# Kernel optimization log

Hardware: AMD Instinct MI355X
Metric: run time of the kernel (lower is better)

## Reference

```python
import jax, jax.numpy as jnp
import numpy as np

B, S, E, H = 1, 4096, 768, 12
D = E // H  # head_dim = 64


def setup_inputs() -> dict:
    key = jax.random.key(0)
    ks = jax.random.split(key, 6)
    scale = 0.02
    x = jax.random.normal(ks[0], (B, S, E), dtype=jnp.float32)
    Wq = jax.random.normal(ks[1], (E, E), dtype=jnp.float32) * scale
    Wk = jax.random.normal(ks[2], (E, E), dtype=jnp.float32) * scale
    Wv = jax.random.normal(ks[3], (E, E), dtype=jnp.float32) * scale
    Wo = jax.random.normal(ks[4], (E, E), dtype=jnp.float32) * scale
    bo = jax.random.normal(ks[5], (E,), dtype=jnp.float32) * scale
    mask = jnp.tril(jnp.ones((S, S), dtype=bool))[None, None]  # [1,1,S,S] causal
    return {"x": x, "Wq": Wq, "Wk": Wk, "Wv": Wv, "Wo": Wo, "bo": bo, "mask": mask}


def reference(x, Wq, Wk, Wv, Wo, bo, mask):
    # projections (torch Linear: y = x @ W.T; here W stored as [E,E] applied as x@W)
    q = jnp.einsum('bse,ef->bsf', x, Wq).reshape(B, S, H, D).transpose(0, 2, 1, 3)
    k = jnp.einsum('bse,ef->bsf', x, Wk).reshape(B, S, H, D).transpose(0, 2, 1, 3)
    v = jnp.einsum('bse,ef->bsf', x, Wv).reshape(B, S, H, D).transpose(0, 2, 1, 3)
    scores = jnp.einsum('bhqd,bhkd->bhqk', q, k) / jnp.sqrt(jnp.float32(D))
    scores = jnp.where(mask, scores, -jnp.inf)
    attn = jax.nn.softmax(scores, axis=-1)  # dropout p=0 -> identity
    ctx = jnp.einsum('bhqk,bhkd->bhqd', attn, v)
    ctx = ctx.transpose(0, 2, 1, 3).reshape(B, S, E)
    return jnp.einsum('bse,ef->bsf', ctx, Wo) + bo
```

## Files before the change

### kernel.cpp

```cpp
#include <hip/hip_runtime.h>
#include <math.h>

#define S 4096
#define E 768
#define H 12
#define Dh 64
#define SCALE2 0.1803368801111204f

typedef short short8 __attribute__((ext_vector_type(8)));
typedef float floatx4 __attribute__((ext_vector_type(4)));

__device__ __forceinline__ unsigned short f2bf(float f) {
    union { float f; unsigned int i; } c; c.f = f;
    unsigned int i = c.i;
    return (unsigned short)((i + 0x7fffu + ((i >> 16) & 1u)) >> 16);
}

__device__ __forceinline__ unsigned int pk_bf16(float lo, float hi) {
#if __has_builtin(__builtin_amdgcn_cvt_pk_bf16_f32)
    typedef __bf16 bf16x2 __attribute__((ext_vector_type(2)));
    union { bf16x2 v; unsigned int u; } c;
    c.v = __builtin_amdgcn_cvt_pk_bf16_f32(lo, hi);
    return c.u;
#else
    union { float f; unsigned int i; } a, b; a.f = lo; b.f = hi;
    return ((a.i + 0x8000u) >> 16) | ((b.i + 0x8000u) & 0xFFFF0000u);
#endif
}

__device__ __forceinline__ unsigned int scale_pk(unsigned int u, float s) {
    union { unsigned int i; float f; } lo, hi;
    lo.i = u << 16; hi.i = u & 0xffff0000u;
    return pk_bf16(lo.f * s, hi.f * s);
}

__device__ __forceinline__ void pk_atomic_add_bf16(unsigned short* addr, unsigned int bits) {
    unsigned long long a = (unsigned long long)addr;
    asm volatile("global_atomic_pk_add_bf16 %0, %1, off" :: "v"(a), "v"(bits) : "memory");
}

__device__ __forceinline__ void gload_lds16(const unsigned short* g, unsigned short* l) {
    __builtin_amdgcn_global_load_lds(
        (const __attribute__((address_space(1))) unsigned int*)g,
        (__attribute__((address_space(3))) unsigned int*)l, 16, 0, 0);
}

__device__ __forceinline__ void pl32swap(unsigned &a, unsigned &b) {
#if __has_builtin(__builtin_amdgcn_permlane32_swap)
    typedef unsigned uint2v __attribute__((ext_vector_type(2)));
    uint2v r = __builtin_amdgcn_permlane32_swap(a, b, false, false);
    a = r[0]; b = r[1];
#else
    asm("s_nop 1\n\tv_permlane32_swap_b32 %0, %1\n\ts_nop 1" : "+v"(a), "+v"(b));
#endif
}
__device__ __forceinline__ void pl16swap(unsigned &a, unsigned &b) {
#if __has_builtin(__builtin_amdgcn_permlane16_swap)
    typedef unsigned uint2v __attribute__((ext_vector_type(2)));
    uint2v r = __builtin_amdgcn_permlane16_swap(a, b, false, false);
    a = r[0]; b = r[1];
#else
    asm("s_nop 1\n\tv_permlane16_swap_b32 %0, %1\n\ts_nop 1" : "+v"(a), "+v"(b));
#endif
}

__device__ __forceinline__ short8 quad_redist(unsigned a0, unsigned a1, unsigned a2, unsigned a3) {
    pl32swap(a0, a2); pl16swap(a0, a2);
    pl32swap(a1, a3); pl16swap(a1, a3);
    union { unsigned u[4]; short8 s; } r;
    r.u[0] = a0; r.u[1] = a1; r.u[2] = a2; r.u[3] = a3;
    return r.s;
}

__global__ __launch_bounds__(256)
void prep_kernel(const float* __restrict__ x, unsigned short* __restrict__ xb,
                 const float* __restrict__ s0, const float* __restrict__ s1,
                 const float* __restrict__ s2, const float* __restrict__ s3,
                 unsigned short* __restrict__ d0, unsigned short* __restrict__ d1,
                 unsigned short* __restrict__ d2, unsigned short* __restrict__ d3,
                 char* __restrict__ zbase) {
    __shared__ unsigned short tile[32][33];
    const int b = blockIdx.x;
    const int tid = threadIdx.x;
    if (b < 2304) {
        int z = b / 576, rem = b - z * 576;
        int bx = rem % 24, by = rem / 24;
        const float* src = (z == 0) ? s0 : (z == 1) ? s1 : (z == 2) ? s2 : s3;
        unsigned short* dst = (z == 0) ? d0 : (z == 1) ? d1 : (z == 2) ? d2 : d3;
        int tx = tid & 31, ty = tid >> 5;
        int xcol = bx * 32 + tx;
        int y0 = by * 32;
        for (int j = ty; j < 32; j += 8)
            tile[j][tx] = f2bf(src[(size_t)(y0 + j) * E + xcol]);
        __syncthreads();
        int x2 = y0 + tx;
        int y2 = bx * 32;
        for (int j = ty; j < 32; j += 8)
            dst[(size_t)(y2 + j) * E + x2] = tile[tx][j];
    } else if (b < 3840) {
        int i = ((b - 2304) * 256 + tid) * 8;
        float4 f0 = *reinterpret_cast<const float4*>(x + i);
        float4 f1 = *reinterpret_cast<const float4*>(x + i + 4);
        unsigned short u[8];
        u[0]=f2bf(f0.x); u[1]=f2bf(f0.y); u[2]=f2bf(f0.z); u[3]=f2bf(f0.w);
        u[4]=f2bf(f1.x); u[5]=f2bf(f1.y); u[6]=f2bf(f1.z); u[7]=f2bf(f1.w);
        *reinterpret_cast<uint4*>(xb + i) = *reinterpret_cast<uint4*>(u);
    } else {
        size_t i = (size_t)(b - 3840) * 16384 + (size_t)tid * 64;
        uint4 z4 = make_uint4(0u, 0u, 0u, 0u);
        *reinterpret_cast<uint4*>(zbase + i)      = z4;
        *reinterpret_cast<uint4*>(zbase + i + 16) = z4;
        *reinterpret_cast<uint4*>(zbase + i + 32) = z4;
        *reinterpret_cast<uint4*>(zbase + i + 48) = z4;
    }
}

__global__ __launch_bounds__(256)
void gemm_qkv(const unsigned short* __restrict__ A,
              const unsigned short* __restrict__ BT,
              unsigned short* __restrict__ Qb, unsigned short* __restrict__ Kb,
              unsigned short* __restrict__ VTb) {
    __shared__ unsigned short Asm[128 * 64];
    __shared__ unsigned short Bsm[128 * 64];
    const int tid  = threadIdx.x;
    const int wave = tid >> 6, lane = tid & 63;
    const int quad = lane >> 4, l16 = lane & 15;
    const int lrow = lane >> 3, lchunk = lane & 7;
    const int bb = blockIdx.x;
    const int xcd = bb & 7, j = bb >> 3;
    const int mt = (xcd >> 1) * 8 + (j & 7);
    const int nt = (xcd & 1) * 9 + (j >> 3);
    const int n0 = nt * 128;
    const int m0 = mt * 128;
    const int aw = wave >> 1, bw = wave & 1;

    floatx4 acc[4][4];
    #pragma unroll
    for (int at = 0; at < 4; at++)
        #pragma unroll
        for (int ct = 0; ct < 4; ct++)
            #pragma unroll
            for (int r = 0; r < 4; r++) acc[at][ct][r] = 0.f;

    for (int k0 = 0; k0 < E; k0 += 64) {
        #pragma unroll
        for (int i = 0; i < 4; i++) {
            int rbase = wave * 32 + i * 8;
            int row   = rbase + lrow;
            int gc    = lchunk ^ (row & 7);
            gload_lds16(&A [(size_t)(m0 + row) * E + k0 + gc * 8], &Asm[rbase * 64]);
            gload_lds16(&BT[(size_t)(n0 + row) * E + k0 + gc * 8], &Bsm[rbase * 64]);
        }
        __syncthreads();
        #pragma unroll
        for (int kk = 0; kk < 2; kk++) {
            const int g = kk * 4 + quad;
            short8 af[4], bfr[4];
            #pragma unroll
            for (int t = 0; t < 4; t++) {
                int ar = aw * 64 + t * 16 + l16;
                af[t]  = *reinterpret_cast<const short8*>(&Asm[ar * 64 + (g ^ (ar & 7)) * 8]);
                int br = bw * 64 + t * 16 + l16;
                bfr[t] = *reinterpret_cast<const short8*>(&Bsm[br * 64 + (g ^ (br & 7)) * 8]);
            }
            #pragma unroll
            for (int at = 0; at < 4; at++)
                #pragma unroll
                for (int ct = 0; ct < 4; ct++)
                    acc[at][ct] = __builtin_amdgcn_mfma_f32_16x16x32_bf16(af[at], bfr[ct], acc[at][ct], 0, 0, 0);
        }
        __syncthreads();
    }

    const int sec = n0 / 768;
    const int nb  = n0 - sec * 768 + bw * 64;
    if (sec == 2) {
        #pragma unroll
        for (int at = 0; at < 4; at++)
            #pragma unroll
            for (int ct = 0; ct < 4; ct++) {
                int nsec = nb + ct * 16 + l16, hh = nsec >> 6, d = nsec & 63;
                int s0i = m0 + aw * 64 + at * 16 + quad * 4;
                uint2 w2;
                w2.x = pk_bf16(acc[at][ct][0], acc[at][ct][1]);
                w2.y = pk_bf16(acc[at][ct][2], acc[at][ct][3]);
                *reinterpret_cast<uint2*>(&VTb[(size_t)hh * Dh * S + (size_t)d * S + s0i]) = w2;
            }
    } else {
        #pragma unroll
        for (int at = 0; at < 4; at++)
            #pragma unroll
            for (int ct = 0; ct < 4; ct++) {
                int nsec = nb + ct * 16 + l16, hh = nsec >> 6, d = nsec & 63;
                #pragma unroll
                for (int r = 0; r < 4; r++) {
                    int s = m0 + aw * 64 + at * 16 + quad * 4 + r;
                    float v = acc[at][ct][r];
                    if (sec == 0) Qb[(size_t)hh * S * Dh + (size_t)s * Dh + d] = f2bf(v * SCALE2);
                    else          Kb[(size_t)hh * S * Dh + (size_t)s * Dh + d] = f2bf(v);
                }
            }
    }
}

__global__ __launch_bounds__(256)
void gemm_out(const unsigned short* __restrict__ ctxp,
              const unsigned short* __restrict__ BT,
              const float* __restrict__ lsumf,
              float* __restrict__ outp, const float* __restrict__ bias) {
    __shared__ unsigned short Asm[128 * 64];
    __shared__ unsigned short Bsm[64 * 64];
    const int tid  = threadIdx.x;
    const int wave = tid >> 6, lane = tid & 63;
    const int quad = lane >> 4, l16 = lane & 15;
    const int lrow = lane >> 3, lchunk = lane & 7;
    const int bb = blockIdx.x;
    const int xcd = bb & 7, j = bb >> 3;
    const int mt = (xcd >> 1) * 8 + (j & 7);
    const int nt = (xcd & 1) * 6 + (j >> 3);
    const int n0 = nt * 64;
    const int m0 = mt * 128;
    const int arow = tid >> 1, ahalf = tid & 1;

    floatx4 acc[2][4];
    #pragma unroll
    for (int at = 0; at < 2; at++)
        #pragma unroll
        for (int ct = 0; ct < 4; ct++)
            #pragma unroll
            for (int r = 0; r < 4; r++) acc[at][ct][r] = 0.f;

    for (int k0 = 0; k0 < E; k0 += 64) {
        {
            const unsigned short* asrc = ctxp + (size_t)(m0 + arow) * E + k0 + ahalf * 32;
            float linv = 1.0f / lsumf[(k0 >> 6) * S + m0 + arow];
            #pragma unroll
            for (int cc = 0; cc < 4; cc++) {
                uint4 u = *reinterpret_cast<const uint4*>(asrc + cc * 8);
                uint4 w;
                w.x = scale_pk(u.x, linv);
                w.y = scale_pk(u.y, linv);
                w.z = scale_pk(u.z, linv);
                w.w = scale_pk(u.w, linv);
                int chunk = ahalf * 4 + cc;
                *reinterpret_cast<uint4*>(&Asm[arow * 64 + (chunk ^ (arow & 7)) * 8]) = w;
            }
        }
        #pragma unroll
        for (int i = 0; i < 2; i++) {
            int rbase = wave * 16 + i * 8;
            int row   = rbase + lrow;
            int gc    = lchunk ^ (row & 7);
            gload_lds16(&BT[(size_t)(n0 + row) * E + k0 + gc * 8], &Bsm[rbase * 64]);
        }
        __syncthreads();
        #pragma unroll
        for (int kk = 0; kk < 2; kk++) {
            const int g = kk * 4 + quad;
            short8 af[2], bfr[4];
            #pragma unroll
            for (int t = 0; t < 2; t++) {
                int ar = wave * 32 + t * 16 + l16;
                af[t] = *reinterpret_cast<const short8*>(&Asm[ar * 64 + (g ^ (ar & 7)) * 8]);
            }
            #pragma unroll
            for (int ct = 0; ct < 4; ct++) {
                int br = ct * 16 + l16;
                bfr[ct] = *reinterpret_cast<const short8*>(&Bsm[br * 64 + (g ^ (br & 7)) * 8]);
            }
            #pragma unroll
            for (int at = 0; at < 2; at++)
                #pragma unroll
                for (int ct = 0; ct < 4; ct++)
                    acc[at][ct] = __builtin_amdgcn_mfma_f32_16x16x32_bf16(af[at], bfr[ct], acc[at][ct], 0, 0, 0);
        }
        __syncthreads();
    }

    #pragma unroll
    for (int at = 0; at < 2; at++)
        #pragma unroll
        for (int ct = 0; ct < 4; ct++) {
            int n = n0 + ct * 16 + l16;
            float bn = bias[n];
            #pragma unroll
            for (int r = 0; r < 4; r++) {
                int s = m0 + wave * 32 + at * 16 + quad * 4 + r;
                outp[(size_t)s * E + n] = acc[at][ct][r] + bn;
            }
        }
}

__global__ __launch_bounds__(512, 4)
void attn_kernel(const unsigned short* __restrict__ Q,
                 const unsigned short* __restrict__ K,
                 const unsigned short* __restrict__ VT,
                 unsigned short* __restrict__ ctxp,
                 float* __restrict__ lsumf) {
    __shared__ unsigned short Ksm[3][64 * 64];
    __shared__ unsigned short Vsm[3][64 * 64];
    const int tid  = threadIdx.x;
    const int wave = tid >> 6, lane = tid & 63;
    const int quad = lane >> 4, l16 = lane & 15;
    const int lrow = lane >> 3, lchunk = lane & 7;

    const int b = blockIdx.x;
    const int w = b / H;
    const int h = b - w * H;
    int Qb, ck, nck;
    if      (w < 16) { Qb = 15 - (w >> 3);              ck = w & 7;  nck = 8; }
    else if (w < 30) { int u = w - 16; Qb = 13 - u / 7;   ck = u % 7; nck = 7; }
    else if (w < 42) { int u = w - 30; Qb = 11 - u / 6;   ck = u % 6; nck = 6; }
    else if (w < 52) { int u = w - 42; Qb = 9  - u / 5;   ck = u % 5; nck = 5; }
    else if (w < 60) { int u = w - 52; Qb = 7 - (u >> 2); ck = u & 3; nck = 4; }
    else if (w < 66) { int u = w - 60; Qb = 5 - u / 3;    ck = u % 3; nck = 3; }
    else if (w < 70) { int u = w - 66; Qb = 3 - (u >> 1); ck = u & 1; nck = 2; }
    else             { Qb = 1 - (w - 70);                 ck = 0;     nck = 1; }
    const int ntiles = 4 * Qb + 4;
    const int kt0 = (ntiles * ck) / nck;
    const int kt1 = (ntiles * (ck + 1)) / nck;

    const int qs = Qb * 256 + wave * 32;

    const unsigned short* Qh = Q  + (size_t)h * S * Dh;
    const unsigned short* Kh = K  + (size_t)h * S * Dh;
    const unsigned short* Vh = VT + (size_t)h * Dh * S;

    short8 bq[2][2];
    #pragma unroll
    for (int st = 0; st < 2; st++)
        #pragma unroll
        for (int c = 0; c < 2; c++)
            bq[st][c] = *reinterpret_cast<const short8*>(
                &Qh[(size_t)(qs + st * 16 + l16) * Dh + c * 32 + quad * 8]);

    float lsum[2] = {0.f, 0.f};
    floatx4 o[2][4];
    #pragma unroll
    for (int st = 0; st < 2; st++)
        #pragma unroll
        for (int ct = 0; ct < 4; ct++)
            #pragma unroll
            for (int r = 0; r < 4; r++) o[st][ct][r] = 0.f;

    auto stage = [&](int kt, int buf) {
        int rbase = wave * 8;
        int row   = rbase + lrow;
        int gc    = lchunk ^ (row & 7);
        gload_lds16(&Kh[(size_t)(kt * 64 + row) * Dh + gc * 8], &Ksm[buf][rbase * 64]);
        gload_lds16(&Vh[(size_t)row * S + kt * 64 + gc * 8],    &Vsm[buf][rbase * 64]);
    };

    stage(kt0, 0);
    stage(kt0 + 1, 1);

    for (int kt = kt0; kt < kt1; kt++) {
        const int cur = (kt - kt0) % 3;
        if (kt + 1 < kt1) { asm volatile("s_waitcnt vmcnt(2)" ::: "memory"); }
        else              { asm volatile("s_waitcnt vmcnt(0)" ::: "memory"); }
        __builtin_amdgcn_sched_barrier(0);
        __builtin_amdgcn_s_barrier();
        __builtin_amdgcn_sched_barrier(0);
        if (kt + 2 < kt1) stage(kt + 2, (cur + 2) % 3);

        if (kt * 64 <= qs + 31) {
            floatx4 sc[2][4];
            #pragma unroll
            for (int st = 0; st < 2; st++)
                #pragma unroll
                for (int ct = 0; ct < 4; ct++)
                    #pragma unroll
                    for (int r = 0; r < 4; r++) sc[st][ct][r] = 0.f;
            __builtin_amdgcn_s_setprio(1);
            #pragma unroll
            for (int c = 0; c < 2; c++)
                #pragma unroll
                for (int ct = 0; ct < 4; ct++) {
                    int kr = ct * 16 + l16;
                    short8 ak = *reinterpret_cast<const short8*>(
                        &Ksm[cur][kr * 64 + ((c * 4 + quad) ^ (kr & 7)) * 8]);
                    sc[0][ct] = __builtin_amdgcn_mfma_f32_16x16x32_bf16(ak, bq[0][c], sc[0][ct], 0, 0, 0);
                    sc[1][ct] = __builtin_amdgcn_mfma_f32_16x16x32_bf16(ak, bq[1][c], sc[1][ct], 0, 0, 0);
                }
            __builtin_amdgcn_s_setprio(0);

            if (kt * 64 + 63 > qs) {
                #pragma unroll
                for (int st = 0; st < 2; st++) {
                    int qrow = qs + st * 16 + l16;
                    #pragma unroll
                    for (int ct = 0; ct < 4; ct++)
                        #pragma unroll
                        for (int r = 0; r < 4; r++) {
                            int kcol = kt * 64 + ct * 16 + quad * 4 + r;
                            if (kcol > qrow) sc[st][ct][r] = -INFINITY;
                        }
                }
            }

            unsigned Dp0[8], Dp1[8];
            #pragma unroll
            for (int ct = 0; ct < 4; ct++) {
                float a0 = __builtin_amdgcn_exp2f(sc[0][ct][0]);
                float a1 = __builtin_amdgcn_exp2f(sc[0][ct][1]);
                float a2 = __builtin_amdgcn_exp2f(sc[0][ct][2]);
                float a3 = __builtin_amdgcn_exp2f(sc[0][ct][3]);
                lsum[0] += a0 + a1 + a2 + a3;
                Dp0[ct * 2 + 0] = pk_bf16(a0, a1);
                Dp0[ct * 2 + 1] = pk_bf16(a2, a3);
                float b0 = __builtin_amdgcn_exp2f(sc[1][ct][0]);
                float b1 = __builtin_amdgcn_exp2f(sc[1][ct][1]);
                float b2 = __builtin_amdgcn_exp2f(sc[1][ct][2]);
                float b3 = __builtin_amdgcn_exp2f(sc[1][ct][3]);
                lsum[1] += b0 + b1 + b2 + b3;
                Dp1[ct * 2 + 0] = pk_bf16(b0, b1);
                Dp1[ct * 2 + 1] = pk_bf16(b2, b3);
            }

            __builtin_amdgcn_s_setprio(1);
            #pragma unroll
            for (int c = 0; c < 2; c++) {
                short8 ap0 = quad_redist(Dp0[4*c+0], Dp0[4*c+1], Dp0[4*c+2], Dp0[4*c+3]);
                short8 ap1 = quad_redist(Dp1[4*c+0], Dp1[4*c+1], Dp1[4*c+2], Dp1[4*c+3]);
                #pragma unroll
                for (int ct = 0; ct < 4; ct++) {
                    int vr = ct * 16 + l16;
                    short8 bv = *reinterpret_cast<const short8*>(
                        &Vsm[cur][vr * 64 + ((c * 4 + quad) ^ (vr & 7)) * 8]);
                    o[0][ct] = __builtin_amdgcn_mfma_f32_16x16x32_bf16(ap0, bv, o[0][ct], 0, 0, 0);
                    o[1][ct] = __builtin_amdgcn_mfma_f32_16x16x32_bf16(ap1, bv, o[1][ct], 0, 0, 0);
                }
            }
            __builtin_amdgcn_s_setprio(0);
        }
    }

    #pragma unroll
    for (int st = 0; st < 2; st++) {
        lsum[st] += __shfl_xor(lsum[st], 16, 64);
        lsum[st] += __shfl_xor(lsum[st], 32, 64);
    }
    if (quad == 0) {
        #pragma unroll
        for (int st = 0; st < 2; st++)
            atomicAdd(&lsumf[h * S + qs + st * 16 + l16], lsum[st]);
    }
    #pragma unroll
    for (int st = 0; st < 2; st++)
        #pragma unroll
        for (int r = 0; r < 4; r++) {
            int s = qs + st * 16 + quad * 4 + r;
            #pragma unroll
            for (int ct = 0; ct < 4; ct++) {
                float v  = o[st][ct][r];
                float vn = __shfl_xor(v, 1, 64);
                if ((l16 & 1) == 0)
                    pk_atomic_add_bf16(&ctxp[(size_t)s * E + h * Dh + ct * 16 + l16],
                                       pk_bf16(v, vn));
            }
        }
}

extern "C" void kernel_launch(void* const* d_in, const int* in_sizes, int n_in,
                              void* d_out, int out_size, void* d_ws, size_t ws_size,
                              hipStream_t stream) {
    const float* x  = (const float*)d_in[0];
    const float* Wq = (const float*)d_in[1];
    const float* Wk = (const float*)d_in[2];
    const float* Wv = (const float*)d_in[3];
    const float* Wo = (const float*)d_in[4];
    const float* bo = (const float*)d_in[5];
    float* out = (float*)d_out;

    char* ws = (char*)d_ws;
    const size_t WT = (size_t)E * E * 2;
    const size_t QB = (size_t)S * E * 2;
    unsigned short* WqT = (unsigned short*)(ws + 0 * WT);
    unsigned short* WkT = (unsigned short*)(ws + 1 * WT);
    unsigned short* WvT = (unsigned short*)(ws + 2 * WT);
    unsigned short* WoT = (unsigned short*)(ws + 3 * WT);
    unsigned short* xb  = (unsigned short*)(ws + 4 * WT + 0 * QB);
    unsigned short* Qbf = (unsigned short*)(ws + 4 * WT + 1 * QB);
    unsigned short* Kbf = (unsigned short*)(ws + 4 * WT + 2 * QB);
    unsigned short* VTb = (unsigned short*)(ws + 4 * WT + 3 * QB);
    unsigned short* ctxp  = (unsigned short*)(ws + 4 * WT + 4 * QB);
    float*          lsumf = (float*)(ws + 4 * WT + 5 * QB);

    prep_kernel<<<4236, 256, 0, stream>>>(
        x, xb, Wq, Wk, Wv, Wo, WqT, WkT, WvT, WoT, (char*)ctxp);

    gemm_qkv<<<576, 256, 0, stream>>>(xb, WqT, Qbf, Kbf, VTb);

    attn_kernel<<<864, 512, 0, stream>>>(Qbf, Kbf, VTb, ctxp, lsumf);

    gemm_out<<<384, 256, 0, stream>>>(ctxp, WoT, lsumf, out, bo);
}
```

Before: 238.6 us.

## Double-buffer LDS tiles in QKV and output projection GEMMs

Both projection GEMMs now use two LDS buffers per operand and prefetch the next K-slice, using explicit vmcnt waits and raw s_barrier instead of __syncthreads. The out-projection GEMM also splits its normalized A load into a register prefetch and a later scale-and-write into the spare buffer. The aim is to hide global-load latency behind MFMA work in these GEMMs. In exchange it doubles LDS use and relies on hand-counted vmcnt values, which are fragile if the compiler reorders or merges loads.

```diff
diff --git a/kernel.cpp b/kernel.cpp
--- a/kernel.cpp
+++ b/kernel.cpp
@@ -120,8 +120,8 @@
               const unsigned short* __restrict__ BT,
               unsigned short* __restrict__ Qb, unsigned short* __restrict__ Kb,
               unsigned short* __restrict__ VTb) {
-    __shared__ unsigned short Asm[128 * 64];
-    __shared__ unsigned short Bsm[128 * 64];
+    __shared__ unsigned short Asm[2][128 * 64];
+    __shared__ unsigned short Bsm[2][128 * 64];
     const int tid  = threadIdx.x;
     const int wave = tid >> 6, lane = tid & 63;
     const int quad = lane >> 4, l16 = lane & 15;
@@ -142,16 +142,31 @@
             #pragma unroll
             for (int r = 0; r < 4; r++) acc[at][ct][r] = 0.f;
 
-    for (int k0 = 0; k0 < E; k0 += 64) {
+    auto stage = [&](int k0, int buf) {
         #pragma unroll
         for (int i = 0; i < 4; i++) {
             int rbase = wave * 32 + i * 8;
             int row   = rbase + lrow;
             int gc    = lchunk ^ (row & 7);
-            gload_lds16(&A [(size_t)(m0 + row) * E + k0 + gc * 8], &Asm[rbase * 64]);
-            gload_lds16(&BT[(size_t)(n0 + row) * E + k0 + gc * 8], &Bsm[rbase * 64]);
-        }
-        __syncthreads();
+            gload_lds16(&A [(size_t)(m0 + row) * E + k0 + gc * 8], &Asm[buf][rbase * 64]);
+            gload_lds16(&BT[(size_t)(n0 + row) * E + k0 + gc * 8], &Bsm[buf][rbase * 64]);
+        }
+    };
+
+    stage(0, 0);
+    stage(64, 1);
+
+    for (int ki = 0; ki < 12; ki++) {
+        const int cur = ki & 1;
+        if (ki < 11) { asm volatile("s_waitcnt vmcnt(8)" ::: "memory"); }
+        else         { asm volatile("s_waitcnt vmcnt(0)" ::: "memory"); }
+        asm volatile("s_waitcnt lgkmcnt(0)" ::: "memory");
+        __builtin_amdgcn_sched_barrier(0);
+        __builtin_amdgcn_s_barrier();
+        __builtin_amdgcn_sched_barrier(0);
+
+        const unsigned short* As = Asm[cur];
+        const unsigned short* Bs = Bsm[cur];
         #pragma unroll
         for (int kk = 0; kk < 2; kk++) {
             const int g = kk * 4 + quad;
@@ -159,9 +174,9 @@
             #pragma unroll
             for (int t = 0; t < 4; t++) {
                 int ar = aw * 64 + t * 16 + l16;
-                af[t]  = *reinterpret_cast<const short8*>(&Asm[ar * 64 + (g ^ (ar & 7)) * 8]);
+                af[t]  = *reinterpret_cast<const short8*>(&As[ar * 64 + (g ^ (ar & 7)) * 8]);
                 int br = bw * 64 + t * 16 + l16;
-                bfr[t] = *reinterpret_cast<const short8*>(&Bsm[br * 64 + (g ^ (br & 7)) * 8]);
+                bfr[t] = *reinterpret_cast<const short8*>(&Bs[br * 64 + (g ^ (br & 7)) * 8]);
             }
             #pragma unroll
             for (int at = 0; at < 4; at++)
@@ -169,7 +184,12 @@
                 for (int ct = 0; ct < 4; ct++)
                     acc[at][ct] = __builtin_amdgcn_mfma_f32_16x16x32_bf16(af[at], bfr[ct], acc[at][ct], 0, 0, 0);
         }
-        __syncthreads();
+
+        if (ki < 10) {
+            __builtin_amdgcn_s_barrier();
+            __builtin_amdgcn_sched_barrier(0);
+            stage((ki + 2) * 64, cur);
+        }
     }
 
     const int sec = n0 / 768;
@@ -208,8 +228,8 @@
               const unsigned short* __restrict__ BT,
               const float* __restrict__ lsumf,
               float* __restrict__ outp, const float* __restrict__ bias) {
-    __shared__ unsigned short Asm[128 * 64];
-    __shared__ unsigned short Bsm[64 * 64];
+    __shared__ unsigned short Asm[2][128 * 64];
+    __shared__ unsigned short Bsm[2][64 * 64];
     const int tid  = threadIdx.x;
     const int wave = tid >> 6, lane = tid & 63;
     const int quad = lane >> 4, l16 = lane & 15;
@@ -230,30 +250,65 @@
             #pragma unroll
             for (int r = 0; r < 4; r++) acc[at][ct][r] = 0.f;
 
-    for (int k0 = 0; k0 < E; k0 += 64) {
-        {
-            const unsigned short* asrc = ctxp + (size_t)(m0 + arow) * E + k0 + ahalf * 32;
-            float linv = 1.0f / lsumf[(k0 >> 6) * S + m0 + arow];
-            #pragma unroll
-            for (int cc = 0; cc < 4; cc++) {
-                uint4 u = *reinterpret_cast<const uint4*>(asrc + cc * 8);
-                uint4 w;
-                w.x = scale_pk(u.x, linv);
-                w.y = scale_pk(u.y, linv);
-                w.z = scale_pk(u.z, linv);
-                w.w = scale_pk(u.w, linv);
-                int chunk = ahalf * 4 + cc;
-                *reinterpret_cast<uint4*>(&Asm[arow * 64 + (chunk ^ (arow & 7)) * 8]) = w;
-            }
-        }
+    uint4 au[4]; float lf;
+    auto loadA = [&](int k0) {
+        const unsigned short* asrc = ctxp + (size_t)(m0 + arow) * E + k0 + ahalf * 32;
+        au[0] = *reinterpret_cast<const uint4*>(asrc + 0);
+        au[1] = *reinterpret_cast<const uint4*>(asrc + 8);
+        au[2] = *reinterpret_cast<const uint4*>(asrc + 16);
+        au[3] = *reinterpret_cast<const uint4*>(asrc + 24);
+        lf = lsumf[(k0 >> 6) * S + m0 + arow];
+    };
+    auto writeA = [&](int buf) {
+        float linv = 1.0f / lf;
+        #pragma unroll
+        for (int cc = 0; cc < 4; cc++) {
+            uint4 w;
+            w.x = scale_pk(au[cc].x, linv);
+            w.y = scale_pk(au[cc].y, linv);
+            w.z = scale_pk(au[cc].z, linv);
+            w.w = scale_pk(au[cc].w, linv);
+            int chunk = ahalf * 4 + cc;
+            *reinterpret_cast<uint4*>(&Asm[buf][arow * 64 + (chunk ^ (arow & 7)) * 8]) = w;
+        }
+    };
+    auto stageB = [&](int k0, int buf) {
         #pragma unroll
         for (int i = 0; i < 2; i++) {
             int rbase = wave * 16 + i * 8;
             int row   = rbase + lrow;
             int gc    = lchunk ^ (row & 7);
-            gload_lds16(&BT[(size_t)(n0 + row) * E + k0 + gc * 8], &Bsm[rbase * 64]);
-        }
-        __syncthreads();
+            gload_lds16(&BT[(size_t)(n0 + row) * E + k0 + gc * 8], &Bsm[buf][rbase * 64]);
+        }
+    };
+
+    loadA(0);
+    __builtin_amdgcn_sched_barrier(0);
+    asm volatile("s_waitcnt vmcnt(0)" ::: "memory");
+    writeA(0);
+    __builtin_amdgcn_sched_barrier(0);
+    stageB(0, 0);
+    __builtin_amdgcn_sched_barrier(0);
+    loadA(64);
+    __builtin_amdgcn_sched_barrier(0);
+
+    for (int ki = 0; ki < 12; ki++) {
+        const int cur = ki & 1, nxt = cur ^ 1;
+        if (ki <= 10) { asm volatile("s_waitcnt vmcnt(5)" ::: "memory"); }
+        else          { asm volatile("s_waitcnt vmcnt(0)" ::: "memory"); }
+        asm volatile("s_waitcnt lgkmcnt(0)" ::: "memory");
+        __builtin_amdgcn_sched_barrier(0);
+        __builtin_amdgcn_s_barrier();
+        __builtin_amdgcn_sched_barrier(0);
+        asm volatile("s_waitcnt vmcnt(0)" ::: "memory");
+        if (ki < 11) writeA(nxt);
+        __builtin_amdgcn_sched_barrier(0);
+        if (ki < 11) stageB((ki + 1) * 64, nxt);
+        if (ki <= 9) loadA((ki + 2) * 64);
+        __builtin_amdgcn_sched_barrier(0);
+
+        const unsigned short* As = Asm[cur];
+        const unsigned short* Bs = Bsm[cur];
         #pragma unroll
         for (int kk = 0; kk < 2; kk++) {
             const int g = kk * 4 + quad;
@@ -261,12 +316,12 @@
             #pragma unroll
             for (int t = 0; t < 2; t++) {
                 int ar = wave * 32 + t * 16 + l16;
-                af[t] = *reinterpret_cast<const short8*>(&Asm[ar * 64 + (g ^ (ar & 7)) * 8]);
+                af[t] = *reinterpret_cast<const short8*>(&As[ar * 64 + (g ^ (ar & 7)) * 8]);
             }
             #pragma unroll
             for (int ct = 0; ct < 4; ct++) {
                 int br = ct * 16 + l16;
-                bfr[ct] = *reinterpret_cast<const short8*>(&Bsm[br * 64 + (g ^ (br & 7)) * 8]);
+                bfr[ct] = *reinterpret_cast<const short8*>(&Bs[br * 64 + (g ^ (br & 7)) * 8]);
             }
             #pragma unroll
             for (int at = 0; at < 2; at++)
@@ -274,7 +329,6 @@
                 for (int ct = 0; ct < 4; ct++)
                     acc[at][ct] = __builtin_amdgcn_mfma_f32_16x16x32_bf16(af[at], bfr[ct], acc[at][ct], 0, 0, 0);
         }
-        __syncthreads();
     }
 
     #pragma unroll
```

Result: faster. 230.3 us (-3.4%).
